# Kernel tuning notes

Measured on AMD Instinct MI355X. Metric: run time of the kernel, lower is better.

The kernel has to match this reference:

```python
import jax, jax.numpy as jnp
import numpy as np
from jax import lax

B, CIN, COUT, H, W = 4, 256, 256, 64, 64
KH = KW = 3
K = KH * KW
GN_GROUPS = 32
EPS = 1e-5


def setup_inputs() -> dict:
    key = jax.random.key(0)
    ks = jax.random.split(key, 6)
    x = jax.random.normal(ks[0], (B, CIN, H, W), jnp.float32)
    # offset predictor conv: 3x3, 18 out channels, with bias (init small so offsets stay near 0)
    offset_w = jax.random.normal(ks[1], (2 * K, CIN, KH, KW), jnp.float32) * 0.01
    offset_b = jax.random.normal(ks[2], (2 * K,), jnp.float32) * 0.01
    # deformable conv weight (no bias), He-ish scale
    deform_w = jax.random.normal(ks[3], (COUT, CIN, KH, KW), jnp.float32) * (1.0 / np.sqrt(CIN * K))
    gn_gamma = jnp.ones((COUT,), jnp.float32)
    gn_beta = jnp.zeros((COUT,), jnp.float32)
    return {"x": x, "offset_w": offset_w, "offset_b": offset_b,
            "deform_w": deform_w, "gn_gamma": gn_gamma, "gn_beta": gn_beta}


def _deform_conv(x, offset, weight):
    """Deformable conv v1, stride=1, pad=1, dil=1, deformable_groups=1.
    x: [B,C,H,W]; offset: [B,2K,H,W] with (dy,dx) per kernel tap; weight: [O,C,3,3].
    """
    b, c, h, w = x.shape
    off = offset.reshape(b, K, 2, h, w)
    # base sampling grid per kernel tap: p = p0 - pad + k
    ky, kx = jnp.meshgrid(jnp.arange(KH), jnp.arange(KW), indexing="ij")
    base_y = (jnp.arange(h, dtype=jnp.float32) - 1.0)[None, :, None] + ky.reshape(K).astype(jnp.float32)[:, None, None]  # [K,H,1]
    base_x = (jnp.arange(w, dtype=jnp.float32) - 1.0)[None, None, :] + kx.reshape(K).astype(jnp.float32)[:, None, None]  # [K,1,W]
    py = base_y[None] + off[:, :, 0]  # [B,K,H,W]
    px = base_x[None] + off[:, :, 1]  # [B,K,H,W]

    y0 = jnp.floor(py)
    x0 = jnp.floor(px)
    ty = py - y0
    tx = px - x0
    y0 = y0.astype(jnp.int32)
    x0 = x0.astype(jnp.int32)

    x_hw = x.transpose(0, 2, 3, 1).reshape(b, h * w, c)  # [B,HW,C]

    def corner(yi, xi, wgt):
        valid = (yi >= 0) & (yi < h) & (xi >= 0) & (xi < w)
        yc = jnp.clip(yi, 0, h - 1)
        xc = jnp.clip(xi, 0, w - 1)
        idx = (yc * w + xc).reshape(b, K * h * w)
        v = jnp.take_along_axis(x_hw, idx[..., None], axis=1)  # [B,KHW,C]
        return v * (wgt * valid.astype(wgt.dtype)).reshape(b, K * h * w, 1)

    samp = (corner(y0, x0, (1 - ty) * (1 - tx))
            + corner(y0, x0 + 1, (1 - ty) * tx)
            + corner(y0 + 1, x0, ty * (1 - tx))
            + corner(y0 + 1, x0 + 1, ty * tx))  # [B,KHW,C]
    samp = samp.reshape(b, K, h, w, c)
    return jnp.einsum("bkhwc,ock->bohw", samp, weight.reshape(weight.shape[0], c, K))


def reference(x, offset_w, offset_b, deform_w, gn_gamma, gn_beta):
    # offset = conv3x3(x) + bias
    offset = lax.conv_general_dilated(
        x, offset_w, window_strides=(1, 1), padding=((1, 1), (1, 1)),
        dimension_numbers=("NCHW", "OIHW", "NCHW")) + offset_b[None, :, None, None]
    out = _deform_conv(x, offset, deform_w)
    # GroupNorm(32, COUT) + ReLU
    b, c, h, w = out.shape
    g = out.reshape(b, GN_GROUPS, (c // GN_GROUPS) * h * w)
    mu = g.mean(axis=2, keepdims=True)
    var = g.var(axis=2, keepdims=True)
    g = (g - mu) * lax.rsqrt(var + EPS)
    out = g.reshape(b, c, h, w) * gn_gamma[None, :, None, None] + gn_beta[None, :, None, None]
    return jax.nn.relu(out)
```

## Files before the change

### kernel.cpp

```cpp
#include <hip/hip_runtime.h>
#include <hip/hip_bf16.h>
#include <stdint.h>


typedef unsigned short u16;
typedef __bf16 bf16x8 __attribute__((ext_vector_type(8)));
typedef float f32x4_t __attribute__((ext_vector_type(4)));

#define HW 4096

__device__ __forceinline__ uint32_t f32_to_bf16_rne(float f) {
  uint32_t u = __builtin_bit_cast(uint32_t, f);
  return (u + 0x7FFFu + ((u >> 16) & 1u)) >> 16;
}
__device__ __forceinline__ float bf_lo(uint32_t u) {
  return __builtin_bit_cast(float, u << 16);
}
__device__ __forceinline__ float bf_hi(uint32_t u) {
  return __builtin_bit_cast(float, u & 0xFFFF0000u);
}

__global__ __launch_bounds__(256) void k_transpose(const float* __restrict__ x,
                                                   u16* __restrict__ xt) {
  __shared__ float tile[32][33];
  int b = blockIdx.z;
  int c0 = blockIdx.y * 32;
  int p0 = blockIdx.x * 32;
  int tx = threadIdx.x, ty = threadIdx.y;
#pragma unroll
  for (int j = 0; j < 32; j += 8)
    tile[ty + j][tx] = x[(b * 256 + c0 + ty + j) * HW + p0 + tx];
  __syncthreads();
  int wid = ty * 32 + tx;
  int cp = wid & 15;
  int pr = wid >> 4;
#pragma unroll
  for (int j = 0; j < 2; j++) {
    int p = pr + j * 16;
    uint32_t lo = f32_to_bf16_rne(tile[cp * 2][p]);
    uint32_t hi = f32_to_bf16_rne(tile[cp * 2 + 1][p]);
    *(uint32_t*)&xt[(b * HW + p0 + p) * 256 + c0 + cp * 2] = lo | (hi << 16);
  }
}

__global__ __launch_bounds__(256) void k_prep_w(const float* __restrict__ wsrc,
                                                u16* __restrict__ warr) {
  int e = blockIdx.x * 256 + threadIdx.x;
  int kk = e & 7, m = (e >> 3) & 255, g = (e >> 11) & 7, kc = e >> 14;
  int cin = (kc & 3) * 64 + g * 8 + kk;
  int tap = kc >> 2;
  float v = wsrc[m * 2304 + cin * 9 + tap];
  warr[e] = (u16)f32_to_bf16_rne(v);
}

__global__ __launch_bounds__(256) void k_prep_owm(const float* __restrict__ ow,
                                                  u16* __restrict__ owm) {
  int e = blockIdx.x * 256 + threadIdx.x;
  int kk = e & 7, m = (e >> 3) & 31, g = (e >> 8) & 7, kc = e >> 11;
  int cin = (kc & 3) * 64 + g * 8 + kk;
  int tap = kc >> 2;
  float v = (m < 18) ? ow[m * 2304 + cin * 9 + tap] : 0.f;
  owm[e] = (u16)f32_to_bf16_rne(v);
}

__global__ __launch_bounds__(256) void k_offmm(
    const u16* __restrict__ xt, const u16* __restrict__ owm,
    const float* __restrict__ ob, int4* __restrict__ midx, float4* __restrict__ mwt) {
  __shared__ u16 b_w[4][1088];
  __shared__ float off_part[4][16][20];
  int tid = threadIdx.x;
  int lane = tid & 63;
  int w = tid >> 6;
  int b = blockIdx.x >> 8;
  int pt = blockIdx.x & 255;
  int p0 = pt * 16;
  int yrow = p0 >> 6;
  int xbase = p0 & 63;

  f32x4_t acc2[2] = {};
  int q = lane & 15;

#pragma unroll 1
  for (int tap = w; tap < 9; tap += 4) {
    int ky = tap / 3, kx = tap % 3;
    int yy = yrow + ky - 1;
    bool vy = (yy >= 0) && (yy < 64);
#pragma unroll
    for (int cc = 0; cc < 4; cc++) {
      int kc = tap * 4 + cc;
#pragma unroll
      for (int i = 0; i < 4; i++) {
        int px = i * 4 + (lane >> 4);
        int xx2 = xbase + px + kx - 1;
        uint2 v = make_uint2(0u, 0u);
        if (vy && xx2 >= 0 && xx2 < 64)
          v = *(const uint2*)&xt[(b * HW + yy * 64 + xx2) * 256 + cc * 64 + q * 4];
        *(uint2*)&b_w[w][(q >> 1) * 136 + px * 8 + (q & 1) * 4] = v;
      }
#pragma unroll
      for (int ks = 0; ks < 2; ks++) {
        int g = ks * 4 + (lane >> 4);
        bf16x8 bfr = *(bf16x8*)&b_w[w][g * 136 + (lane & 15) * 8];
#pragma unroll
        for (int im = 0; im < 2; im++) {
          bf16x8 af = *(const bf16x8*)&owm[kc * 2048 + g * 256 + (im * 16 + (lane & 15)) * 8];
          acc2[im] = __builtin_amdgcn_mfma_f32_16x16x32_bf16(af, bfr, acc2[im], 0, 0, 0);
        }
      }
    }
  }
  {
    int px = lane & 15, rq = lane >> 4;
#pragma unroll
    for (int im = 0; im < 2; im++)
#pragma unroll
      for (int r = 0; r < 4; r++) {
        int oc = im * 16 + rq * 4 + r;
        if (oc < 18) off_part[w][px][oc] = acc2[im][r];
      }
  }
  __syncthreads();
  if (tid < 144) {
    int tap = tid >> 4;
    int px = tid & 15;
    float dy = off_part[0][px][2 * tap] + off_part[1][px][2 * tap] +
               off_part[2][px][2 * tap] + off_part[3][px][2 * tap] + ob[2 * tap];
    float dx = off_part[0][px][2 * tap + 1] + off_part[1][px][2 * tap + 1] +
               off_part[2][px][2 * tap + 1] + off_part[3][px][2 * tap + 1] + ob[2 * tap + 1];
    int ky = tap / 3, kx = tap % 3;
    int p = p0 + px;
    int yq = p >> 6, xq = p & 63;
    float py = (float)(yq - 1 + ky) + dy;
    float pxx = (float)(xq - 1 + kx) + dx;
    float y0f = floorf(py), x0f = floorf(pxx);
    float ty = py - y0f, tx = pxx - x0f;
    int y0 = (int)y0f, x0 = (int)x0f;
    int y1 = y0 + 1, x1 = x0 + 1;
    float wy0 = 1.f - ty, wy1 = ty, wx0 = 1.f - tx, wx1 = tx;
    bool vy0 = (y0 >= 0) && (y0 < 64), vy1 = (y1 >= 0) && (y1 < 64);
    bool vx0 = (x0 >= 0) && (x0 < 64), vx1 = (x1 >= 0) && (x1 < 64);
    int cy0 = min(max(y0, 0), 63), cy1 = min(max(y1, 0), 63);
    int cx0 = min(max(x0, 0), 63), cx1 = min(max(x1, 0), 63);
    int base = b * HW;
    int4 ci;
    ci.x = (base + cy0 * 64 + cx0) * 256;
    ci.y = (base + cy0 * 64 + cx1) * 256;
    ci.z = (base + cy1 * 64 + cx0) * 256;
    ci.w = (base + cy1 * 64 + cx1) * 256;
    float4 mw;
    mw.x = wy0 * wx0 * ((vy0 && vx0) ? 1.f : 0.f);
    mw.y = wy0 * wx1 * ((vy0 && vx1) ? 1.f : 0.f);
    mw.z = wy1 * wx0 * ((vy1 && vx0) ? 1.f : 0.f);
    mw.w = wy1 * wx1 * ((vy1 && vx1) ? 1.f : 0.f);
    int mi = (b * 9 + tap) * HW + p;
    midx[mi] = ci;
    mwt[mi] = mw;
  }
}

__global__ __launch_bounds__(256) void k_gemm(
    const u16* __restrict__ xt, const u16* __restrict__ warr,
    const int4* __restrict__ midx, const float4* __restrict__ mwt,
    float* __restrict__ out) {
  __shared__ u16 b_s[2][1088];
  int tid = threadIdx.x;
  int lane = tid & 63;
  int wm = tid >> 6;
  int b = blockIdx.x >> 8;
  int pt = blockIdx.x & 255;
  int p0 = pt * 16;
  int q = tid & 15;
  int pxb = tid >> 4;

  f32x4_t acc4[4] = {};

#pragma unroll 1
  for (int tap = 0; tap < 9; tap++) {
    int mi = (b * 9 + tap) * HW + p0 + pxb;
    int4 ci = midx[mi];
    float4 mw4 = mwt[mi];
#pragma unroll
    for (int cc = 0; cc < 4; cc++) {
      int kc = tap * 4 + cc;
      int e = cc * 64 + q * 4;
      uint2 c0v = *(const uint2*)&xt[ci.x + e];
      uint2 c1v = *(const uint2*)&xt[ci.y + e];
      uint2 c2v = *(const uint2*)&xt[ci.z + e];
      uint2 c3v = *(const uint2*)&xt[ci.w + e];
      float r0 = mw4.x * bf_lo(c0v.x) + mw4.y * bf_lo(c1v.x) + mw4.z * bf_lo(c2v.x) + mw4.w * bf_lo(c3v.x);
      float r1 = mw4.x * bf_hi(c0v.x) + mw4.y * bf_hi(c1v.x) + mw4.z * bf_hi(c2v.x) + mw4.w * bf_hi(c3v.x);
      float r2 = mw4.x * bf_lo(c0v.y) + mw4.y * bf_lo(c1v.y) + mw4.z * bf_lo(c2v.y) + mw4.w * bf_lo(c3v.y);
      float r3 = mw4.x * bf_hi(c0v.y) + mw4.y * bf_hi(c1v.y) + mw4.z * bf_hi(c2v.y) + mw4.w * bf_hi(c3v.y);
      uint2 u;
      u.x = f32_to_bf16_rne(r0) | (f32_to_bf16_rne(r1) << 16);
      u.y = f32_to_bf16_rne(r2) | (f32_to_bf16_rne(r3) << 16);
      *(uint2*)&b_s[kc & 1][(q >> 1) * 136 + pxb * 8 + (q & 1) * 4] = u;
      __syncthreads();
#pragma unroll
      for (int ks = 0; ks < 2; ks++) {
        int g = ks * 4 + (lane >> 4);
        bf16x8 bfr = *(bf16x8*)&b_s[kc & 1][g * 136 + (lane & 15) * 8];
        const u16* abase = warr + kc * 16384 + g * 2048 + (wm * 64 + (lane & 15)) * 8;
#pragma unroll
        for (int im = 0; im < 4; im++) {
          bf16x8 af = *(const bf16x8*)&abase[im * 128];
          acc4[im] = __builtin_amdgcn_mfma_f32_16x16x32_bf16(af, bfr, acc4[im], 0, 0, 0);
        }
      }
    }
  }
  int rq = lane >> 4;
  int n = p0 + (lane & 15);
#pragma unroll
  for (int im = 0; im < 4; im++) {
#pragma unroll
    for (int r = 0; r < 4; r++) {
      int m = wm * 64 + im * 16 + rq * 4 + r;
      out[(b * 256 + m) * HW + n] = acc4[im][r];
    }
  }
}

__global__ __launch_bounds__(256) void k_gn_part(const float* __restrict__ out,
                                                 float2* __restrict__ part) {
  int blk = blockIdx.x;
  int bg = blk >> 2, qt = blk & 3;
  const float4* base = (const float4*)(out + (size_t)bg * 32768 + (size_t)qt * 8192);
  int tid = threadIdx.x;
  float s = 0.f, ss = 0.f;
#pragma unroll
  for (int i = 0; i < 8; i++) {
    float4 v = base[tid + i * 256];
    s += v.x + v.y + v.z + v.w;
    ss += v.x * v.x + v.y * v.y + v.z * v.z + v.w * v.w;
  }
#pragma unroll
  for (int m = 1; m < 64; m <<= 1) {
    s += __shfl_xor(s, m);
    ss += __shfl_xor(ss, m);
  }
  __shared__ float ls[4], lss[4];
  int wv = tid >> 6, lane = tid & 63;
  if (lane == 0) { ls[wv] = s; lss[wv] = ss; }
  __syncthreads();
  if (tid == 0)
    part[blk] = make_float2(ls[0] + ls[1] + ls[2] + ls[3],
                            lss[0] + lss[1] + lss[2] + lss[3]);
}

__global__ __launch_bounds__(256) void k_gn_apply(float* __restrict__ out,
                                                  const float2* __restrict__ part,
                                                  const float* __restrict__ gamma,
                                                  const float* __restrict__ beta) {
  __shared__ float sga, sbe;
  int gid = blockIdx.x * 256 + threadIdx.x;
  int c = (gid >> 10) & 255;
  int bb = gid >> 18;
  if (threadIdx.x == 0) {
    int p4 = (bb * 32 + (c >> 3)) * 4;
    float s = 0.f, ss = 0.f;
#pragma unroll
    for (int j = 0; j < 4; j++) {
      float2 p = part[p4 + j];
      s += p.x;
      ss += p.y;
    }
    float mu = s / 32768.f;
    float var = ss / 32768.f - mu * mu;
    float rs = rsqrtf(var + 1e-5f);
    float ga = gamma[c] * rs;
    sga = ga;
    sbe = beta[c] - mu * ga;
  }
  __syncthreads();
  float ga = sga, be = sbe;
  float4 v = ((const float4*)out)[gid];
  v.x = fmaxf(v.x * ga + be, 0.f);
  v.y = fmaxf(v.y * ga + be, 0.f);
  v.z = fmaxf(v.z * ga + be, 0.f);
  v.w = fmaxf(v.w * ga + be, 0.f);
  ((float4*)out)[gid] = v;
}

extern "C" void kernel_launch(void* const* d_in, const int* in_sizes, int n_in,
                              void* d_out, int out_size, void* d_ws, size_t ws_size,
                              hipStream_t stream) {
  const float* x = (const float*)d_in[0];
  const float* offset_w = (const float*)d_in[1];
  const float* offset_b = (const float*)d_in[2];
  const float* deform_w = (const float*)d_in[3];
  const float* gn_gamma = (const float*)d_in[4];
  const float* gn_beta = (const float*)d_in[5];
  float* out = (float*)d_out;
  char* ws = (char*)d_ws;

  u16* xt = (u16*)ws;
  int4* midx = (int4*)(ws + 8388608);
  float4* mwt = (float4*)(ws + 10747904);
  u16* warr = (u16*)(ws + 13107200);
  u16* owm = (u16*)(ws + 14286848);
  float2* part = (float2*)(ws + 14434304);

  k_transpose<<<dim3(128, 8, 4), dim3(32, 8), 0, stream>>>(x, xt);
  k_prep_w<<<dim3(2304), dim3(256), 0, stream>>>(deform_w, warr);
  k_prep_owm<<<dim3(288), dim3(256), 0, stream>>>(offset_w, owm);
  k_offmm<<<dim3(1024), dim3(256), 0, stream>>>(xt, owm, offset_b, midx, mwt);
  k_gemm<<<dim3(1024), dim3(256), 0, stream>>>(xt, warr, midx, mwt, out);
  k_gn_part<<<dim3(512), dim3(256), 0, stream>>>(out, part);
  k_gn_apply<<<dim3(4096), dim3(256), 0, stream>>>(out, part, gn_gamma, gn_beta);
}
```

Before: 180.0 us.

## Fuse offset conv and deformable GEMM into one kernel with 32-pixel tiles

Merges the offset-predicting conv and the deformable sampling GEMM into a single kernel, so the bilinear indices and weights stay in shared memory instead of going through global workspace. Each block now covers 32 pixels instead of 16, so every weight fragment loaded from global memory feeds two MFMAs, which halves A-operand traffic per output. The cost is fewer blocks (512), more shared memory and more registers per block, which may lower occupancy. The offset conv is also computed for 32 pixels per block.

```diff
diff --git a/kernel.cpp b/kernel.cpp
--- a/kernel.cpp
+++ b/kernel.cpp
@@ -63,70 +63,82 @@
   owm[e] = (u16)f32_to_bf16_rne(v);
 }
 
-__global__ __launch_bounds__(256) void k_offmm(
-    const u16* __restrict__ xt, const u16* __restrict__ owm,
-    const float* __restrict__ ob, int4* __restrict__ midx, float4* __restrict__ mwt) {
-  __shared__ u16 b_w[4][1088];
-  __shared__ float off_part[4][16][20];
+__global__ __launch_bounds__(256) void k_conv(
+    const u16* __restrict__ xt, const u16* __restrict__ warr,
+    const u16* __restrict__ owm, const float* __restrict__ ob,
+    float* __restrict__ out) {
+  __shared__ char smem[27136];
+  u16* stage = (u16*)smem;
+  float* off_part = (float*)(smem + 16896);
+  int4* ci_s = (int4*)smem;
+  float4* mw_s = (float4*)(smem + 4608);
+  u16* b_s = (u16*)(smem + 16896);
+
   int tid = threadIdx.x;
   int lane = tid & 63;
-  int w = tid >> 6;
-  int b = blockIdx.x >> 8;
-  int pt = blockIdx.x & 255;
-  int p0 = pt * 16;
-  int yrow = p0 >> 6;
-  int xbase = p0 & 63;
-
-  f32x4_t acc2[2] = {};
-  int q = lane & 15;
-
+  int wm = tid >> 6;
+  int b = blockIdx.x >> 7;
+  int pt = blockIdx.x & 127;
+  int p0 = pt * 32;
+  int yrow = p0 >> 6, xbase = p0 & 63;
+
+  {
+    u16* st = stage + wm * 2112;
+    int q = lane & 15, pq = lane >> 4;
+    f32x4_t a2[2][2] = {};
 #pragma unroll 1
-  for (int tap = w; tap < 9; tap += 4) {
-    int ky = tap / 3, kx = tap % 3;
-    int yy = yrow + ky - 1;
-    bool vy = (yy >= 0) && (yy < 64);
-#pragma unroll
-    for (int cc = 0; cc < 4; cc++) {
-      int kc = tap * 4 + cc;
-#pragma unroll
-      for (int i = 0; i < 4; i++) {
-        int px = i * 4 + (lane >> 4);
-        int xx2 = xbase + px + kx - 1;
-        uint2 v = make_uint2(0u, 0u);
-        if (vy && xx2 >= 0 && xx2 < 64)
-          v = *(const uint2*)&xt[(b * HW + yy * 64 + xx2) * 256 + cc * 64 + q * 4];
-        *(uint2*)&b_w[w][(q >> 1) * 136 + px * 8 + (q & 1) * 4] = v;
-      }
-#pragma unroll
-      for (int ks = 0; ks < 2; ks++) {
-        int g = ks * 4 + (lane >> 4);
-        bf16x8 bfr = *(bf16x8*)&b_w[w][g * 136 + (lane & 15) * 8];
-#pragma unroll
-        for (int im = 0; im < 2; im++) {
-          bf16x8 af = *(const bf16x8*)&owm[kc * 2048 + g * 256 + (im * 16 + (lane & 15)) * 8];
-          acc2[im] = __builtin_amdgcn_mfma_f32_16x16x32_bf16(af, bfr, acc2[im], 0, 0, 0);
+    for (int tap = wm; tap < 9; tap += 4) {
+      int ky = tap / 3, kx = tap % 3;
+      int yy = yrow + ky - 1;
+      bool vy = (yy >= 0) && (yy < 64);
+#pragma unroll
+      for (int cc = 0; cc < 4; cc++) {
+        int kc = tap * 4 + cc;
+#pragma unroll
+        for (int i = 0; i < 8; i++) {
+          int px = i * 4 + pq;
+          int xx2 = xbase + px + kx - 1;
+          uint2 v = make_uint2(0u, 0u);
+          if (vy && xx2 >= 0 && xx2 < 64)
+            v = *(const uint2*)&xt[(b * HW + yy * 64 + xx2) * 256 + cc * 64 + q * 4];
+          *(uint2*)&st[(q >> 1) * 264 + px * 8 + (q & 1) * 4] = v;
         }
+#pragma unroll
+        for (int ks = 0; ks < 2; ks++) {
+          int g = ks * 4 + pq;
+          const u16* ab = owm + kc * 2048 + g * 256;
+#pragma unroll
+          for (int s = 0; s < 2; s++) {
+            bf16x8 bfr = *(bf16x8*)&st[g * 264 + (s * 16 + q) * 8];
+#pragma unroll
+            for (int im = 0; im < 2; im++) {
+              bf16x8 af = *(const bf16x8*)&ab[(im * 16 + q) * 8];
+              a2[s][im] = __builtin_amdgcn_mfma_f32_16x16x32_bf16(af, bfr, a2[s][im], 0, 0, 0);
+            }
+          }
+        }
       }
     }
-  }
-  {
-    int px = lane & 15, rq = lane >> 4;
-#pragma unroll
-    for (int im = 0; im < 2; im++)
-#pragma unroll
-      for (int r = 0; r < 4; r++) {
-        int oc = im * 16 + rq * 4 + r;
-        if (oc < 18) off_part[w][px][oc] = acc2[im][r];
-      }
-  }
-  __syncthreads();
-  if (tid < 144) {
-    int tap = tid >> 4;
-    int px = tid & 15;
-    float dy = off_part[0][px][2 * tap] + off_part[1][px][2 * tap] +
-               off_part[2][px][2 * tap] + off_part[3][px][2 * tap] + ob[2 * tap];
-    float dx = off_part[0][px][2 * tap + 1] + off_part[1][px][2 * tap + 1] +
-               off_part[2][px][2 * tap + 1] + off_part[3][px][2 * tap + 1] + ob[2 * tap + 1];
+#pragma unroll
+    for (int s = 0; s < 2; s++)
+#pragma unroll
+      for (int im = 0; im < 2; im++)
+#pragma unroll
+        for (int r = 0; r < 4; r++) {
+          int oc = im * 16 + pq * 4 + r;
+          if (oc < 18) off_part[(wm * 32 + s * 16 + q) * 20 + oc] = a2[s][im][r];
+        }
+  }
+  __syncthreads();
+  for (int it = tid; it < 288; it += 256) {
+    int tap = it >> 5;
+    int px = it & 31;
+    float dy = ob[2 * tap], dx = ob[2 * tap + 1];
+#pragma unroll
+    for (int wv = 0; wv < 4; wv++) {
+      dy += off_part[(wv * 32 + px) * 20 + 2 * tap];
+      dx += off_part[(wv * 32 + px) * 20 + 2 * tap + 1];
+    }
     int ky = tap / 3, kx = tap % 3;
     int p = p0 + px;
     int yq = p >> 6, xq = p & 63;
@@ -152,72 +164,79 @@
     mw.y = wy0 * wx1 * ((vy0 && vx1) ? 1.f : 0.f);
     mw.z = wy1 * wx0 * ((vy1 && vx0) ? 1.f : 0.f);
     mw.w = wy1 * wx1 * ((vy1 && vx1) ? 1.f : 0.f);
-    int mi = (b * 9 + tap) * HW + p;
-    midx[mi] = ci;
-    mwt[mi] = mw;
-  }
-}
-
-__global__ __launch_bounds__(256) void k_gemm(
-    const u16* __restrict__ xt, const u16* __restrict__ warr,
-    const int4* __restrict__ midx, const float4* __restrict__ mwt,
-    float* __restrict__ out) {
-  __shared__ u16 b_s[2][1088];
-  int tid = threadIdx.x;
-  int lane = tid & 63;
-  int wm = tid >> 6;
-  int b = blockIdx.x >> 8;
-  int pt = blockIdx.x & 255;
-  int p0 = pt * 16;
-  int q = tid & 15;
-  int pxb = tid >> 4;
-
-  f32x4_t acc4[4] = {};
-
+    ci_s[it] = ci;
+    mw_s[it] = mw;
+  }
+  __syncthreads();
+
+  int q = tid & 15, pxb = (tid >> 4) & 15;
+  f32x4_t acc[2][4] = {};
 #pragma unroll 1
   for (int tap = 0; tap < 9; tap++) {
-    int mi = (b * 9 + tap) * HW + p0 + pxb;
-    int4 ci = midx[mi];
-    float4 mw4 = mwt[mi];
+    int4 ci0 = ci_s[tap * 32 + pxb];
+    int4 ci1 = ci_s[tap * 32 + 16 + pxb];
+    float4 mw0 = mw_s[tap * 32 + pxb];
+    float4 mw1 = mw_s[tap * 32 + 16 + pxb];
 #pragma unroll
     for (int cc = 0; cc < 4; cc++) {
       int kc = tap * 4 + cc;
       int e = cc * 64 + q * 4;
-      uint2 c0v = *(const uint2*)&xt[ci.x + e];
-      uint2 c1v = *(const uint2*)&xt[ci.y + e];
-      uint2 c2v = *(const uint2*)&xt[ci.z + e];
-      uint2 c3v = *(const uint2*)&xt[ci.w + e];
-      float r0 = mw4.x * bf_lo(c0v.x) + mw4.y * bf_lo(c1v.x) + mw4.z * bf_lo(c2v.x) + mw4.w * bf_lo(c3v.x);
-      float r1 = mw4.x * bf_hi(c0v.x) + mw4.y * bf_hi(c1v.x) + mw4.z * bf_hi(c2v.x) + mw4.w * bf_hi(c3v.x);
-      float r2 = mw4.x * bf_lo(c0v.y) + mw4.y * bf_lo(c1v.y) + mw4.z * bf_lo(c2v.y) + mw4.w * bf_lo(c3v.y);
-      float r3 = mw4.x * bf_hi(c0v.y) + mw4.y * bf_hi(c1v.y) + mw4.z * bf_hi(c2v.y) + mw4.w * bf_hi(c3v.y);
-      uint2 u;
-      u.x = f32_to_bf16_rne(r0) | (f32_to_bf16_rne(r1) << 16);
-      u.y = f32_to_bf16_rne(r2) | (f32_to_bf16_rne(r3) << 16);
-      *(uint2*)&b_s[kc & 1][(q >> 1) * 136 + pxb * 8 + (q & 1) * 4] = u;
+      u16* bb = b_s + (kc & 1) * 2176;
+      {
+        uint2 c0v = *(const uint2*)&xt[ci0.x + e];
+        uint2 c1v = *(const uint2*)&xt[ci0.y + e];
+        uint2 c2v = *(const uint2*)&xt[ci0.z + e];
+        uint2 c3v = *(const uint2*)&xt[ci0.w + e];
+        float r0 = mw0.x * bf_lo(c0v.x) + mw0.y * bf_lo(c1v.x) + mw0.z * bf_lo(c2v.x) + mw0.w * bf_lo(c3v.x);
+        float r1 = mw0.x * bf_hi(c0v.x) + mw0.y * bf_hi(c1v.x) + mw0.z * bf_hi(c2v.x) + mw0.w * bf_hi(c3v.x);
+        float r2 = mw0.x * bf_lo(c0v.y) + mw0.y * bf_lo(c1v.y) + mw0.z * bf_lo(c2v.y) + mw0.w * bf_lo(c3v.y);
+        float r3 = mw0.x * bf_hi(c0v.y) + mw0.y * bf_hi(c1v.y) + mw0.z * bf_hi(c2v.y) + mw0.w * bf_hi(c3v.y);
+        uint2 u;
+        u.x = f32_to_bf16_rne(r0) | (f32_to_bf16_rne(r1) << 16);
+        u.y = f32_to_bf16_rne(r2) | (f32_to_bf16_rne(r3) << 16);
+        *(uint2*)&bb[(q >> 1) * 136 + pxb * 8 + (q & 1) * 4] = u;
+      }
+      {
+        uint2 c0v = *(const uint2*)&xt[ci1.x + e];
+        uint2 c1v = *(const uint2*)&xt[ci1.y + e];
+        uint2 c2v = *(const uint2*)&xt[ci1.z + e];
+        uint2 c3v = *(const uint2*)&xt[ci1.w + e];
+        float r0 = mw1.x * bf_lo(c0v.x) + mw1.y * bf_lo(c1v.x) + mw1.z * bf_lo(c2v.x) + mw1.w * bf_lo(c3v.x);
+        float r1 = mw1.x * bf_hi(c0v.x) + mw1.y * bf_hi(c1v.x) + mw1.z * bf_hi(c2v.x) + mw1.w * bf_hi(c3v.x);
+        float r2 = mw1.x * bf_lo(c0v.y) + mw1.y * bf_lo(c1v.y) + mw1.z * bf_lo(c2v.y) + mw1.w * bf_lo(c3v.y);
+        float r3 = mw1.x * bf_hi(c0v.y) + mw1.y * bf_hi(c1v.y) + mw1.z * bf_hi(c2v.y) + mw1.w * bf_hi(c3v.y);
+        uint2 u;
+        u.x = f32_to_bf16_rne(r0) | (f32_to_bf16_rne(r1) << 16);
+        u.y = f32_to_bf16_rne(r2) | (f32_to_bf16_rne(r3) << 16);
+        *(uint2*)&bb[1088 + (q >> 1) * 136 + pxb * 8 + (q & 1) * 4] = u;
+      }
       __syncthreads();
 #pragma unroll
       for (int ks = 0; ks < 2; ks++) {
         int g = ks * 4 + (lane >> 4);
-        bf16x8 bfr = *(bf16x8*)&b_s[kc & 1][g * 136 + (lane & 15) * 8];
-        const u16* abase = warr + kc * 16384 + g * 2048 + (wm * 64 + (lane & 15)) * 8;
+        bf16x8 b0 = *(bf16x8*)&bb[g * 136 + (lane & 15) * 8];
+        bf16x8 b1 = *(bf16x8*)&bb[1088 + g * 136 + (lane & 15) * 8];
+        const u16* ab = warr + kc * 16384 + g * 2048 + (wm * 64 + (lane & 15)) * 8;
 #pragma unroll
         for (int im = 0; im < 4; im++) {
-          bf16x8 af = *(const bf16x8*)&abase[im * 128];
-          acc4[im] = __builtin_amdgcn_mfma_f32_16x16x32_bf16(af, bfr, acc4[im], 0, 0, 0);
+          bf16x8 af = *(const bf16x8*)&ab[im * 128];
+          acc[0][im] = __builtin_amdgcn_mfma_f32_16x16x32_bf16(af, b0, acc[0][im], 0, 0, 0);
+          acc[1][im] = __builtin_amdgcn_mfma_f32_16x16x32_bf16(af, b1, acc[1][im], 0, 0, 0);
         }
       }
     }
   }
   int rq = lane >> 4;
-  int n = p0 + (lane & 15);
-#pragma unroll
-  for (int im = 0; im < 4; im++) {
-#pragma unroll
-    for (int r = 0; r < 4; r++) {
-      int m = wm * 64 + im * 16 + rq * 4 + r;
-      out[(b * 256 + m) * HW + n] = acc4[im][r];
-    }
+#pragma unroll
+  for (int s = 0; s < 2; s++) {
+    int n = p0 + s * 16 + (lane & 15);
+#pragma unroll
+    for (int im = 0; im < 4; im++)
+#pragma unroll
+      for (int r = 0; r < 4; r++) {
+        int m = wm * 64 + im * 16 + rq * 4 + r;
+        out[(b * 256 + m) * HW + n] = acc[s][im][r];
+      }
   }
 }
 
@@ -295,17 +314,14 @@
   char* ws = (char*)d_ws;
 
   u16* xt = (u16*)ws;
-  int4* midx = (int4*)(ws + 8388608);
-  float4* mwt = (float4*)(ws + 10747904);
-  u16* warr = (u16*)(ws + 13107200);
-  u16* owm = (u16*)(ws + 14286848);
-  float2* part = (float2*)(ws + 14434304);
+  u16* warr = (u16*)(ws + 8388608);
+  u16* owm = (u16*)(ws + 9568256);
+  float2* part = (float2*)(ws + 9715712);
 
   k_transpose<<<dim3(128, 8, 4), dim3(32, 8), 0, stream>>>(x, xt);
   k_prep_w<<<dim3(2304), dim3(256), 0, stream>>>(deform_w, warr);
   k_prep_owm<<<dim3(288), dim3(256), 0, stream>>>(offset_w, owm);
-  k_offmm<<<dim3(1024), dim3(256), 0, stream>>>(xt, owm, offset_b, midx, mwt);
-  k_gemm<<<dim3(1024), dim3(256), 0, stream>>>(xt, warr, midx, mwt, out);
+  k_conv<<<dim3(512), dim3(256), 0, stream>>>(xt, warr, owm, offset_b, out);
   k_gn_part<<<dim3(512), dim3(256), 0, stream>>>(out, part);
   k_gn_apply<<<dim3(4096), dim3(256), 0, stream>>>(out, part, gn_gamma, gn_beta);
 }
```

After: 172.1 us. 1.05x faster.
